# Optimization experiments

Measured on AMD Instinct MI355X. Metric: run time of the kernel, lower is better.

## Reference

```python
import jax, jax.numpy as jnp
import numpy as np

NB_HEAD = 8
SIZE_PER_HEAD = 64
EMB = 512  # word embedding dim; output_dim = NB_HEAD*SIZE_PER_HEAD = 512
B, S = 8, 4096


def setup_inputs() -> dict:
    key = jax.random.key(0)
    ks = jax.random.split(key, 8)
    return {
        "Q_seq": jax.random.normal(ks[0], (B, S, EMB), dtype=jnp.float32),
        "K_seq": jax.random.normal(ks[1], (B, S, EMB), dtype=jnp.float32),
        "V_seq": jax.random.normal(ks[2], (B, S, EMB), dtype=jnp.float32),
        "Q_len": jax.random.randint(ks[3], (B, 1), 0, S, dtype=jnp.int32),
        "V_len": jax.random.randint(ks[4], (B, 1), 0, SIZE_PER_HEAD, dtype=jnp.int32),
        "WQ": jax.random.normal(ks[5], (EMB, NB_HEAD * SIZE_PER_HEAD), dtype=jnp.float32),
        "WK": jax.random.normal(ks[6], (EMB, NB_HEAD * SIZE_PER_HEAD), dtype=jnp.float32),
        "WV": jax.random.normal(ks[7], (EMB, NB_HEAD * SIZE_PER_HEAD), dtype=jnp.float32),
    }


def _proj_heads(x, W):
    # [B,S,E] @ [E,H*d] -> [B,H,S,d]
    y = jnp.einsum('bse,eo->bso', x, W)
    y = y.reshape(y.shape[0], y.shape[1], NB_HEAD, SIZE_PER_HEAD)
    return jnp.transpose(y, (0, 2, 1, 3))


def reference(Q_seq, K_seq, V_seq, Q_len, V_len, WQ, WK, WV):
    H, d = NB_HEAD, SIZE_PER_HEAD
    Q = _proj_heads(Q_seq, WQ)  # [B,H,S,d]
    K = _proj_heads(K_seq, WK)
    V = _proj_heads(V_seq, WV)

    A = (Q * K) / jnp.asarray(d, Q.dtype) ** 0.5  # elementwise, [B,H,S,d]

    # TF code transposes A to [B,d,S,H] and masks along axis 1 (size d) using
    # V_len, then transposes back. Equivalent: additive mask on the LAST axis.
    vmask = jax.nn.one_hot(V_len[:, 0], d, dtype=A.dtype)       # [B,d]
    vmask = 1.0 - jnp.cumsum(vmask, axis=1)                      # [B,d]
    A = A - (1.0 - vmask)[:, None, None, :] * 1e12

    A = jax.nn.softmax(A, axis=-1)  # softmax over d (last axis), as tf.nn.softmax

    O = A * V                              # [B,H,S,d]
    O = jnp.transpose(O, (0, 2, 1, 3))     # [B,S,H,d]
    O = O.reshape(O.shape[0], O.shape[1], H * d)  # [B,S,H*d]

    # multiplicative mask over sequence axis using Q_len
    qmask = jax.nn.one_hot(Q_len[:, 0], O.shape[1], dtype=O.dtype)  # [B,S]
    qmask = 1.0 - jnp.cumsum(qmask, axis=1)
    return O * qmask[:, :, None]
```

## Files before the change

### kernel.cpp

```cpp
#include <hip/hip_runtime.h>

typedef unsigned short u16;
typedef _Float16 f16;
typedef _Float16 f16x4 __attribute__((ext_vector_type(4)));
typedef _Float16 f16x8 __attribute__((ext_vector_type(8)));
typedef float    f32x4 __attribute__((ext_vector_type(4)));

#define BATCH 8
#define SEQ   4096
#define EMB   512
#define NCOL  512

__global__ __launch_bounds__(256) void prep_w(
    const float* __restrict__ Wq, const float* __restrict__ Wk,
    const float* __restrict__ Wv, u16* __restrict__ out)
{
  __shared__ u16 tile[64][65];
  const int z = blockIdx.z;
  const float* in = (z < 2) ? Wq : (z < 4) ? Wk : Wv;
  const bool lo = (z == 1 || z == 3);
  u16* o = out + (size_t)z * EMB * NCOL;
  const int r0 = blockIdx.y * 64, c0 = blockIdx.x * 64;
  const int tx = threadIdx.x, ty = threadIdx.y;
#pragma unroll
  for (int i = 0; i < 16; ++i) {
    const int r = ty * 16 + i;
    const float x = in[(size_t)(r0 + r) * NCOL + (c0 + tx)];
    const f16 h = (f16)x;
    const f16 v = lo ? (f16)((x - (float)h) * 16.0f) : h;
    tile[r][tx] = __builtin_bit_cast(u16, v);
  }
  __syncthreads();
#pragma unroll
  for (int i = 0; i < 16; ++i) {
    const int rr = ty * 16 + i;
    o[(size_t)(c0 + rr) * EMB + (r0 + tx)] = tile[tx][rr];
  }
}

#define PLANE 2048
#define BUFSZ (5*PLANE)

__global__ __launch_bounds__(512, 4) void fused_attn(
    const float* __restrict__ Xq, const float* __restrict__ Xk,
    const float* __restrict__ Xv,
    const int* __restrict__ Qlen, const int* __restrict__ Vlen,
    const u16* __restrict__ Wt,
    float* __restrict__ out)
{
  const int b  = blockIdx.z;
  const int s0 = blockIdx.x * 64;
  const int c0 = blockIdx.y * 128;
  const int qlen = Qlen[b];
  const int t = threadIdx.x;

  if (s0 >= qlen) {
    const f32x4 z4 = {0.f, 0.f, 0.f, 0.f};
#pragma unroll
    for (int it = 0; it < 4; ++it) {
      const int f4  = it * 512 + t;
      const int row = f4 >> 5;
      const int col = (f4 & 31) * 4;
      *(f32x4*)(out + (size_t)(b * SEQ + s0 + row) * NCOL + c0 + col) = z4;
    }
    return;
  }
  const int vlen = Vlen[b];
  const int vl = (vlen == 0) ? 64 : vlen;

  __shared__ f16 smem[2 * BUFSZ] __attribute__((aligned(16)));

  const int w    = t >> 6;
  const int lane = t & 63;
  const int quad = lane >> 4;
  const int l15  = lane & 15;

  const int    srow = t >> 3;
  const int    sj   = t & 7;
  const size_t xg   = (size_t)(b * SEQ + s0 + srow) * EMB + sj * 4;
  const int    swo  = srow * 32 + (((sj >> 1) ^ ((srow >> 1) & 3)) * 8) + (sj & 1) * 4;

  const size_t wb = (size_t)(c0 + w * 16 + l15) * EMB + quad * 8;
  const u16* Wqh_g = Wt                + wb;
  const u16* Wql_g = Wt + 1 * EMB*NCOL + wb;
  const u16* Wkh_g = Wt + 2 * EMB*NCOL + wb;
  const u16* Wkl_g = Wt + 3 * EMB*NCOL + wb;
  const u16* Wv_g  = Wt + 4 * EMB*NCOL + wb;

  const int swz = (l15 >> 1) & 3;
  const int ao  = l15 * 32 + ((quad ^ swz) * 8);

  f32x4 accQ[4], accK[4], accV[4];
#pragma unroll
  for (int rt = 0; rt < 4; ++rt) {
    const f32x4 z = {0.f, 0.f, 0.f, 0.f};
    accQ[rt] = z; accK[rt] = z; accV[rt] = z;
  }

  f32x4 rq, rk, rv;

#define LOADX(TT) do { \
    rq = *(const f32x4*)(Xq + xg + (TT) * 32); \
    rk = *(const f32x4*)(Xk + xg + (TT) * 32); \
    rv = *(const f32x4*)(Xv + xg + (TT) * 32); \
  } while (0)

#define STAGE(BOFS) do { \
    f16* p_ = smem + (BOFS); \
    f16x4 qh_, ql_, kh_, kl_, vh_; \
    _Pragma("unroll") \
    for (int j = 0; j < 4; ++j) { \
      const float xq_ = rq[j]; const f16 qhh_ = (f16)xq_; \
      qh_[j] = qhh_; ql_[j] = (f16)((xq_ - (float)qhh_) * 16.0f); \
      const float xk_ = rk[j]; const f16 khh_ = (f16)xk_; \
      kh_[j] = khh_; kl_[j] = (f16)((xk_ - (float)khh_) * 16.0f); \
      vh_[j] = (f16)rv[j]; \
    } \
    *(f16x4*)(p_ + 0 * PLANE + swo) = qh_; \
    *(f16x4*)(p_ + 1 * PLANE + swo) = ql_; \
    *(f16x4*)(p_ + 2 * PLANE + swo) = kh_; \
    *(f16x4*)(p_ + 3 * PLANE + swo) = kl_; \
    *(f16x4*)(p_ + 4 * PLANE + swo) = vh_; \
  } while (0)

#define COMPUTE(BOFS, KK) do { \
    const f16* p_ = smem + (BOFS); \
    const int kk_ = (KK); \
     \
    { \
      const f16x8 bh_ = *(const f16x8*)(Wqh_g + kk_); \
      const f16x8 bl_ = *(const f16x8*)(Wql_g + kk_); \
      f16x8 b4_; \
      _Pragma("unroll") \
      for (int jj = 0; jj < 8; ++jj) b4_[jj] = bh_[jj] * (f16)0.0625f; \
      _Pragma("unroll") \
      for (int rt = 0; rt < 4; ++rt) { \
        const int ao_ = ao + rt * 512; \
        const f16x8 ah_ = *(const f16x8*)(p_ + 0 * PLANE + ao_); \
        const f16x8 al_ = *(const f16x8*)(p_ + 1 * PLANE + ao_); \
        f16x8 a4_; \
        _Pragma("unroll") \
        for (int jj = 0; jj < 8; ++jj) a4_[jj] = ah_[jj] * (f16)0.0625f; \
        accQ[rt] = __builtin_amdgcn_mfma_f32_16x16x32_f16(ah_, bh_, accQ[rt], 0, 0, 0); \
        accQ[rt] = __builtin_amdgcn_mfma_f32_16x16x32_f16(a4_, bl_, accQ[rt], 0, 0, 0); \
        accQ[rt] = __builtin_amdgcn_mfma_f32_16x16x32_f16(al_, b4_, accQ[rt], 0, 0, 0); \
      } \
    } \
     \
    { \
      const f16x8 bh_ = *(const f16x8*)(Wkh_g + kk_); \
      const f16x8 bl_ = *(const f16x8*)(Wkl_g + kk_); \
      f16x8 b4_; \
      _Pragma("unroll") \
      for (int jj = 0; jj < 8; ++jj) b4_[jj] = bh_[jj] * (f16)0.0625f; \
      _Pragma("unroll") \
      for (int rt = 0; rt < 4; ++rt) { \
        const int ao_ = ao + rt * 512; \
        const f16x8 ah_ = *(const f16x8*)(p_ + 2 * PLANE + ao_); \
        const f16x8 al_ = *(const f16x8*)(p_ + 3 * PLANE + ao_); \
        f16x8 a4_; \
        _Pragma("unroll") \
        for (int jj = 0; jj < 8; ++jj) a4_[jj] = ah_[jj] * (f16)0.0625f; \
        accK[rt] = __builtin_amdgcn_mfma_f32_16x16x32_f16(ah_, bh_, accK[rt], 0, 0, 0); \
        accK[rt] = __builtin_amdgcn_mfma_f32_16x16x32_f16(a4_, bl_, accK[rt], 0, 0, 0); \
        accK[rt] = __builtin_amdgcn_mfma_f32_16x16x32_f16(al_, b4_, accK[rt], 0, 0, 0); \
      } \
    } \
     \
    { \
      const f16x8 bv_ = *(const f16x8*)(Wv_g + kk_); \
      _Pragma("unroll") \
      for (int rt = 0; rt < 4; ++rt) { \
        const f16x8 av_ = *(const f16x8*)(p_ + 4 * PLANE + ao + rt * 512); \
        accV[rt] = __builtin_amdgcn_mfma_f32_16x16x32_f16(av_, bv_, accV[rt], 0, 0, 0); \
      } \
    } \
  } while (0)

  LOADX(0);
  STAGE(0);
  __syncthreads();

#pragma unroll 1
  for (int tt = 0; tt < 16; tt += 2) {
    LOADX(tt + 1);
    COMPUTE(0, tt * 32);
    STAGE(BUFSZ);
    __syncthreads();
    if (tt < 14) LOADX(tt + 2);
    COMPUTE(BUFSZ, (tt + 1) * 32);
    if (tt < 14) STAGE(0);
    __syncthreads();
  }

#undef LOADX
#undef STAGE
#undef COMPUTE

  const float scale = 0.125f;
  float* smf = (float*)smem;

  float eA[4][4];

#pragma unroll
  for (int rt = 0; rt < 4; ++rt) {
#pragma unroll
    for (int r = 0; r < 4; ++r) {
      const float a = accQ[rt][r] * accK[rt][r] * scale;
      const bool msk = ((w & 3) * 16 + l15) < vl;
      float mx = msk ? a : -3.0e38f;
#pragma unroll
      for (int off = 1; off < 16; off <<= 1) mx = fmaxf(mx, __shfl_xor(mx, off));
      const float e = msk ? __expf(a - mx) : 0.0f;
      eA[rt][r] = e;
      float sum = e;
#pragma unroll
      for (int off = 1; off < 16; off <<= 1) sum += __shfl_xor(sum, off);
      const int row = rt * 16 + quad * 4 + r;
      if (l15 == 0) {
        smf[(w * 64 + row) * 2 + 0] = mx;
        smf[(w * 64 + row) * 2 + 1] = sum;
      }
    }
  }
  __syncthreads();

  const int wbase = w & 4;
#pragma unroll
  for (int rt = 0; rt < 4; ++rt) {
#pragma unroll
    for (int r = 0; r < 4; ++r) {
      const int row = rt * 16 + quad * 4 + r;
      const int s   = s0 + row;
      float pm[4], ps[4];
      float M = -3.0e38f;
#pragma unroll
      for (int j = 0; j < 4; ++j) {
        pm[j] = smf[((wbase + j) * 64 + row) * 2 + 0];
        ps[j] = smf[((wbase + j) * 64 + row) * 2 + 1];
        M = fmaxf(M, pm[j]);
      }
      float S = 0.f;
#pragma unroll
      for (int j = 0; j < 4; ++j) S += ps[j] * __expf(pm[j] - M);
      const float qm = (s < qlen) ? 1.0f : 0.0f;
      const float f  = __expf(pm[w & 3] - M) * qm / S;
      const size_t ob = (size_t)(b * SEQ + s) * NCOL + c0 + w * 16 + l15;
      out[ob] = eA[rt][r] * f * accV[rt][r];
    }
  }
}

extern "C" void kernel_launch(void* const* d_in, const int* in_sizes, int n_in,
                              void* d_out, int out_size, void* d_ws, size_t ws_size,
                              hipStream_t stream) {
  const float* Xq   = (const float*)d_in[0];
  const float* Xk   = (const float*)d_in[1];
  const float* Xv   = (const float*)d_in[2];
  const int*   Qlen = (const int*)d_in[3];
  const int*   Vlen = (const int*)d_in[4];
  const float* Wq   = (const float*)d_in[5];
  const float* Wk   = (const float*)d_in[6];
  const float* Wv   = (const float*)d_in[7];
  u16*   Wt  = (u16*)d_ws;
  float* out = (float*)d_out;

  dim3 pg(8, 8, 5), pb(64, 4, 1);
  prep_w<<<pg, pb, 0, stream>>>(Wq, Wk, Wv, Wt);

  dim3 g(SEQ / 64, NCOL / 128, BATCH), blk(512, 1, 1);
  fused_attn<<<g, blk, 0, stream>>>(Xq, Xk, Xv, Qlen, Vlen, Wt, out);
}
```

Before: 372.5 us.

## Use persistent blocks with atomic tile scheduler and drop split-precision rescaling

Turns the fused attention kernel into a persistent-block design: 1024 blocks pull tile indices from a global atomic counter, which is reset by an extra tiny kernel. The goal is to balance load, because tiles past Q_len finish almost immediately while full tiles do all the matmul work. It also removes the ×16 / ×1/16 scaling on the low halves of the split-fp16 operands, which saves the per-iteration vector multiplies and pre-scaled copies. The trade-offs are an extra kernel launch, an atomic and a barrier per tile, and a possible loss of accuracy in the low parts, which may now underflow in fp16.

```diff
diff --git a/kernel.cpp b/kernel.cpp
--- a/kernel.cpp
+++ b/kernel.cpp
@@ -1,6 +1,7 @@
 #include <hip/hip_runtime.h>
 
 typedef unsigned short u16;
+typedef unsigned int   u32;
 typedef _Float16 f16;
 typedef _Float16 f16x4 __attribute__((ext_vector_type(4)));
 typedef _Float16 f16x8 __attribute__((ext_vector_type(8)));
@@ -10,6 +11,7 @@
 #define SEQ   4096
 #define EMB   512
 #define NCOL  512
+#define NTILES 2048
 
 __global__ __launch_bounds__(256) void prep_w(
     const float* __restrict__ Wq, const float* __restrict__ Wk,
@@ -27,7 +29,7 @@
     const int r = ty * 16 + i;
     const float x = in[(size_t)(r0 + r) * NCOL + (c0 + tx)];
     const f16 h = (f16)x;
-    const f16 v = lo ? (f16)((x - (float)h) * 16.0f) : h;
+    const f16 v = lo ? (f16)(x - (float)h) : h;
     tile[r][tx] = __builtin_bit_cast(u16, v);
   }
   __syncthreads();
@@ -38,6 +40,8 @@
   }
 }
 
+__global__ void reset_cnt(u32* cnt) { if (threadIdx.x == 0) *cnt = 0; }
+
 #define PLANE 2048
 #define BUFSZ (5*PLANE)
 
@@ -46,207 +50,200 @@
     const float* __restrict__ Xv,
     const int* __restrict__ Qlen, const int* __restrict__ Vlen,
     const u16* __restrict__ Wt,
-    float* __restrict__ out)
+    float* __restrict__ out, u32* cnt, const int dyn)
 {
-  const int b  = blockIdx.z;
-  const int s0 = blockIdx.x * 64;
-  const int c0 = blockIdx.y * 128;
-  const int qlen = Qlen[b];
   const int t = threadIdx.x;
 
-  if (s0 >= qlen) {
-    const f32x4 z4 = {0.f, 0.f, 0.f, 0.f};
-#pragma unroll
-    for (int it = 0; it < 4; ++it) {
-      const int f4  = it * 512 + t;
-      const int row = f4 >> 5;
-      const int col = (f4 & 31) * 4;
-      *(f32x4*)(out + (size_t)(b * SEQ + s0 + row) * NCOL + c0 + col) = z4;
-    }
-    return;
-  }
-  const int vlen = Vlen[b];
-  const int vl = (vlen == 0) ? 64 : vlen;
-
   __shared__ f16 smem[2 * BUFSZ] __attribute__((aligned(16)));
+  int* slot = (int*)((char*)smem + 2 * BUFSZ * 2 - 4);
 
   const int w    = t >> 6;
   const int lane = t & 63;
   const int quad = lane >> 4;
   const int l15  = lane & 15;
 
-  const int    srow = t >> 3;
-  const int    sj   = t & 7;
-  const size_t xg   = (size_t)(b * SEQ + s0 + srow) * EMB + sj * 4;
-  const int    swo  = srow * 32 + (((sj >> 1) ^ ((srow >> 1) & 3)) * 8) + (sj & 1) * 4;
-
-  const size_t wb = (size_t)(c0 + w * 16 + l15) * EMB + quad * 8;
-  const u16* Wqh_g = Wt                + wb;
-  const u16* Wql_g = Wt + 1 * EMB*NCOL + wb;
-  const u16* Wkh_g = Wt + 2 * EMB*NCOL + wb;
-  const u16* Wkl_g = Wt + 3 * EMB*NCOL + wb;
-  const u16* Wv_g  = Wt + 4 * EMB*NCOL + wb;
+  const int srow = t >> 3;
+  const int sj   = t & 7;
+  const int sk4  = sj * 4;
+  const int swo  = srow * 32 + (((sj >> 1) ^ ((srow >> 1) & 3)) * 8) + (sj & 1) * 4;
 
   const int swz = (l15 >> 1) & 3;
   const int ao  = l15 * 32 + ((quad ^ swz) * 8);
 
-  f32x4 accQ[4], accK[4], accV[4];
-#pragma unroll
-  for (int rt = 0; rt < 4; ++rt) {
-    const f32x4 z = {0.f, 0.f, 0.f, 0.f};
-    accQ[rt] = z; accK[rt] = z; accV[rt] = z;
-  }
-
-  f32x4 rq, rk, rv;
+  const float scale = 0.125f;
+  int tile_static = (int)blockIdx.x;
+
+  for (;;) {
+    if (t == 0) {
+      const int nt = dyn ? (int)atomicAdd(cnt, 1u) : tile_static;
+      tile_static = NTILES;
+      *slot = nt;
+    }
+    __syncthreads();
+    const int tile = __builtin_amdgcn_readfirstlane(*slot);
+    if (tile >= NTILES) break;
+
+    const int s0 = (tile & 63) * 64;
+    const int c0 = ((tile >> 6) & 3) * 128;
+    const int b  = tile >> 8;
+    const int qlen = Qlen[b];
+
+    if (s0 >= qlen) {
+      const f32x4 z4 = {0.f, 0.f, 0.f, 0.f};
+#pragma unroll
+      for (int it = 0; it < 4; ++it) {
+        const int f4  = it * 512 + t;
+        const int row = f4 >> 5;
+        const int col = (f4 & 31) * 4;
+        *(f32x4*)(out + (size_t)(b * SEQ + s0 + row) * NCOL + c0 + col) = z4;
+      }
+      continue;
+    }
+    const int vlen = Vlen[b];
+    const int vl = (vlen == 0) ? 64 : vlen;
+
+    const size_t xg = (size_t)(b * SEQ + s0 + srow) * EMB + sk4;
+    const size_t wb = (size_t)(c0 + w * 16 + l15) * EMB + quad * 8;
+    const u16* Wqh_g = Wt                + wb;
+    const u16* Wql_g = Wt + 1 * EMB*NCOL + wb;
+    const u16* Wkh_g = Wt + 2 * EMB*NCOL + wb;
+    const u16* Wkl_g = Wt + 3 * EMB*NCOL + wb;
+    const u16* Wv_g  = Wt + 4 * EMB*NCOL + wb;
+
+    f32x4 accQ[4], accK[4], accV[4];
+#pragma unroll
+    for (int rt = 0; rt < 4; ++rt) {
+      const f32x4 z = {0.f, 0.f, 0.f, 0.f};
+      accQ[rt] = z; accK[rt] = z; accV[rt] = z;
+    }
+
+    f32x4 rq, rk, rv;
 
 #define LOADX(TT) do { \
-    rq = *(const f32x4*)(Xq + xg + (TT) * 32); \
-    rk = *(const f32x4*)(Xk + xg + (TT) * 32); \
-    rv = *(const f32x4*)(Xv + xg + (TT) * 32); \
-  } while (0)
+      rq = *(const f32x4*)(Xq + xg + (TT) * 32); \
+      rk = *(const f32x4*)(Xk + xg + (TT) * 32); \
+      rv = *(const f32x4*)(Xv + xg + (TT) * 32); \
+    } while (0)
 
 #define STAGE(BOFS) do { \
-    f16* p_ = smem + (BOFS); \
-    f16x4 qh_, ql_, kh_, kl_, vh_; \
-    _Pragma("unroll") \
-    for (int j = 0; j < 4; ++j) { \
-      const float xq_ = rq[j]; const f16 qhh_ = (f16)xq_; \
-      qh_[j] = qhh_; ql_[j] = (f16)((xq_ - (float)qhh_) * 16.0f); \
-      const float xk_ = rk[j]; const f16 khh_ = (f16)xk_; \
-      kh_[j] = khh_; kl_[j] = (f16)((xk_ - (float)khh_) * 16.0f); \
-      vh_[j] = (f16)rv[j]; \
-    } \
-    *(f16x4*)(p_ + 0 * PLANE + swo) = qh_; \
-    *(f16x4*)(p_ + 1 * PLANE + swo) = ql_; \
-    *(f16x4*)(p_ + 2 * PLANE + swo) = kh_; \
-    *(f16x4*)(p_ + 3 * PLANE + swo) = kl_; \
-    *(f16x4*)(p_ + 4 * PLANE + swo) = vh_; \
-  } while (0)
+      f16* p_ = smem + (BOFS); \
+      f16x4 qh_, ql_, kh_, kl_, vh_; \
+      _Pragma("unroll") \
+      for (int j = 0; j < 4; ++j) { \
+        const float xq_ = rq[j]; const f16 qhh_ = (f16)xq_; \
+        qh_[j] = qhh_; ql_[j] = (f16)(xq_ - (float)qhh_); \
+        const float xk_ = rk[j]; const f16 khh_ = (f16)xk_; \
+        kh_[j] = khh_; kl_[j] = (f16)(xk_ - (float)khh_); \
+        vh_[j] = (f16)rv[j]; \
+      } \
+      *(f16x4*)(p_ + 0 * PLANE + swo) = qh_; \
+      *(f16x4*)(p_ + 1 * PLANE + swo) = ql_; \
+      *(f16x4*)(p_ + 2 * PLANE + swo) = kh_; \
+      *(f16x4*)(p_ + 3 * PLANE + swo) = kl_; \
+      *(f16x4*)(p_ + 4 * PLANE + swo) = vh_; \
+    } while (0)
 
 #define COMPUTE(BOFS, KK) do { \
-    const f16* p_ = smem + (BOFS); \
-    const int kk_ = (KK); \
-     \
-    { \
-      const f16x8 bh_ = *(const f16x8*)(Wqh_g + kk_); \
-      const f16x8 bl_ = *(const f16x8*)(Wql_g + kk_); \
-      f16x8 b4_; \
-      _Pragma("unroll") \
-      for (int jj = 0; jj < 8; ++jj) b4_[jj] = bh_[jj] * (f16)0.0625f; \
+      const f16* p_ = smem + (BOFS); \
+      const f16x8 bqh_ = *(const f16x8*)(Wqh_g + (KK)); \
+      const f16x8 bql_ = *(const f16x8*)(Wql_g + (KK)); \
+      const f16x8 bkh_ = *(const f16x8*)(Wkh_g + (KK)); \
+      const f16x8 bkl_ = *(const f16x8*)(Wkl_g + (KK)); \
+      const f16x8 bv_  = *(const f16x8*)(Wv_g  + (KK)); \
       _Pragma("unroll") \
       for (int rt = 0; rt < 4; ++rt) { \
         const int ao_ = ao + rt * 512; \
         const f16x8 ah_ = *(const f16x8*)(p_ + 0 * PLANE + ao_); \
         const f16x8 al_ = *(const f16x8*)(p_ + 1 * PLANE + ao_); \
-        f16x8 a4_; \
-        _Pragma("unroll") \
-        for (int jj = 0; jj < 8; ++jj) a4_[jj] = ah_[jj] * (f16)0.0625f; \
-        accQ[rt] = __builtin_amdgcn_mfma_f32_16x16x32_f16(ah_, bh_, accQ[rt], 0, 0, 0); \
-        accQ[rt] = __builtin_amdgcn_mfma_f32_16x16x32_f16(a4_, bl_, accQ[rt], 0, 0, 0); \
-        accQ[rt] = __builtin_amdgcn_mfma_f32_16x16x32_f16(al_, b4_, accQ[rt], 0, 0, 0); \
-      } \
-    } \
-     \
-    { \
-      const f16x8 bh_ = *(const f16x8*)(Wkh_g + kk_); \
-      const f16x8 bl_ = *(const f16x8*)(Wkl_g + kk_); \
-      f16x8 b4_; \
-      _Pragma("unroll") \
-      for (int jj = 0; jj < 8; ++jj) b4_[jj] = bh_[jj] * (f16)0.0625f; \
+        accQ[rt] = __builtin_amdgcn_mfma_f32_16x16x32_f16(ah_, bqh_, accQ[rt], 0, 0, 0); \
+        accQ[rt] = __builtin_amdgcn_mfma_f32_16x16x32_f16(ah_, bql_, accQ[rt], 0, 0, 0); \
+        accQ[rt] = __builtin_amdgcn_mfma_f32_16x16x32_f16(al_, bqh_, accQ[rt], 0, 0, 0); \
+      } \
       _Pragma("unroll") \
       for (int rt = 0; rt < 4; ++rt) { \
         const int ao_ = ao + rt * 512; \
         const f16x8 ah_ = *(const f16x8*)(p_ + 2 * PLANE + ao_); \
         const f16x8 al_ = *(const f16x8*)(p_ + 3 * PLANE + ao_); \
-        f16x8 a4_; \
-        _Pragma("unroll") \
-        for (int jj = 0; jj < 8; ++jj) a4_[jj] = ah_[jj] * (f16)0.0625f; \
-        accK[rt] = __builtin_amdgcn_mfma_f32_16x16x32_f16(ah_, bh_, accK[rt], 0, 0, 0); \
-        accK[rt] = __builtin_amdgcn_mfma_f32_16x16x32_f16(a4_, bl_, accK[rt], 0, 0, 0); \
-        accK[rt] = __builtin_amdgcn_mfma_f32_16x16x32_f16(al_, b4_, accK[rt], 0, 0, 0); \
-      } \
-    } \
-     \
-    { \
-      const f16x8 bv_ = *(const f16x8*)(Wv_g + kk_); \
+        accK[rt] = __builtin_amdgcn_mfma_f32_16x16x32_f16(ah_, bkh_, accK[rt], 0, 0, 0); \
+        accK[rt] = __builtin_amdgcn_mfma_f32_16x16x32_f16(ah_, bkl_, accK[rt], 0, 0, 0); \
+        accK[rt] = __builtin_amdgcn_mfma_f32_16x16x32_f16(al_, bkh_, accK[rt], 0, 0, 0); \
+      } \
       _Pragma("unroll") \
       for (int rt = 0; rt < 4; ++rt) { \
         const f16x8 av_ = *(const f16x8*)(p_ + 4 * PLANE + ao + rt * 512); \
         accV[rt] = __builtin_amdgcn_mfma_f32_16x16x32_f16(av_, bv_, accV[rt], 0, 0, 0); \
       } \
-    } \
-  } while (0)
-
-  LOADX(0);
-  STAGE(0);
-  __syncthreads();
+    } while (0)
+
+    LOADX(0);
+    STAGE(0);
+    __syncthreads();
 
 #pragma unroll 1
-  for (int tt = 0; tt < 16; tt += 2) {
-    LOADX(tt + 1);
-    COMPUTE(0, tt * 32);
-    STAGE(BUFSZ);
-    __syncthreads();
-    if (tt < 14) LOADX(tt + 2);
-    COMPUTE(BUFSZ, (tt + 1) * 32);
-    if (tt < 14) STAGE(0);
-    __syncthreads();
-  }
+    for (int tt = 0; tt < 16; tt += 2) {
+      LOADX(tt + 1);
+      COMPUTE(0, tt * 32);
+      STAGE(BUFSZ);
+      __syncthreads();
+      if (tt < 14) LOADX(tt + 2);
+      COMPUTE(BUFSZ, (tt + 1) * 32);
+      if (tt < 14) STAGE(0);
+      __syncthreads();
+    }
 
 #undef LOADX
 #undef STAGE
 #undef COMPUTE
 
-  const float scale = 0.125f;
-  float* smf = (float*)smem;
-
-  float eA[4][4];
-
-#pragma unroll
-  for (int rt = 0; rt < 4; ++rt) {
-#pragma unroll
-    for (int r = 0; r < 4; ++r) {
-      const float a = accQ[rt][r] * accK[rt][r] * scale;
-      const bool msk = ((w & 3) * 16 + l15) < vl;
-      float mx = msk ? a : -3.0e38f;
-#pragma unroll
-      for (int off = 1; off < 16; off <<= 1) mx = fmaxf(mx, __shfl_xor(mx, off));
-      const float e = msk ? __expf(a - mx) : 0.0f;
-      eA[rt][r] = e;
-      float sum = e;
-#pragma unroll
-      for (int off = 1; off < 16; off <<= 1) sum += __shfl_xor(sum, off);
-      const int row = rt * 16 + quad * 4 + r;
-      if (l15 == 0) {
-        smf[(w * 64 + row) * 2 + 0] = mx;
-        smf[(w * 64 + row) * 2 + 1] = sum;
+    float* smf = (float*)smem;
+    float eA[4][4];
+
+#pragma unroll
+    for (int rt = 0; rt < 4; ++rt) {
+#pragma unroll
+      for (int r = 0; r < 4; ++r) {
+        const float a = accQ[rt][r] * accK[rt][r] * scale;
+        const bool msk = ((w & 3) * 16 + l15) < vl;
+        float mx = msk ? a : -3.0e38f;
+#pragma unroll
+        for (int off = 1; off < 16; off <<= 1) mx = fmaxf(mx, __shfl_xor(mx, off));
+        const float e = msk ? __expf(a - mx) : 0.0f;
+        eA[rt][r] = e;
+        float sum = e;
+#pragma unroll
+        for (int off = 1; off < 16; off <<= 1) sum += __shfl_xor(sum, off);
+        const int row = rt * 16 + quad * 4 + r;
+        if (l15 == 0) {
+          smf[(w * 64 + row) * 2 + 0] = mx;
+          smf[(w * 64 + row) * 2 + 1] = sum;
+        }
       }
     }
-  }
-  __syncthreads();
-
-  const int wbase = w & 4;
-#pragma unroll
-  for (int rt = 0; rt < 4; ++rt) {
-#pragma unroll
-    for (int r = 0; r < 4; ++r) {
-      const int row = rt * 16 + quad * 4 + r;
-      const int s   = s0 + row;
-      float pm[4], ps[4];
-      float M = -3.0e38f;
-#pragma unroll
-      for (int j = 0; j < 4; ++j) {
-        pm[j] = smf[((wbase + j) * 64 + row) * 2 + 0];
-        ps[j] = smf[((wbase + j) * 64 + row) * 2 + 1];
-        M = fmaxf(M, pm[j]);
+    __syncthreads();
+
+    const int wbase = w & 4;
+#pragma unroll
+    for (int rt = 0; rt < 4; ++rt) {
+#pragma unroll
+      for (int r = 0; r < 4; ++r) {
+        const int row = rt * 16 + quad * 4 + r;
+        const int s   = s0 + row;
+        float pm[4], ps[4];
+        float M = -3.0e38f;
+#pragma unroll
+        for (int j = 0; j < 4; ++j) {
+          pm[j] = smf[((wbase + j) * 64 + row) * 2 + 0];
+          ps[j] = smf[((wbase + j) * 64 + row) * 2 + 1];
+          M = fmaxf(M, pm[j]);
+        }
+        float S = 0.f;
+#pragma unroll
+        for (int j = 0; j < 4; ++j) S += ps[j] * __expf(pm[j] - M);
+        const float qm = (s < qlen) ? 1.0f : 0.0f;
+        const float f  = __expf(pm[w & 3] - M) * qm / S;
+        const size_t ob = (size_t)(b * SEQ + s) * NCOL + c0 + w * 16 + l15;
+        out[ob] = eA[rt][r] * f * accV[rt][r];
       }
-      float S = 0.f;
-#pragma unroll
-      for (int j = 0; j < 4; ++j) S += ps[j] * __expf(pm[j] - M);
-      const float qm = (s < qlen) ? 1.0f : 0.0f;
-      const float f  = __expf(pm[w & 3] - M) * qm / S;
-      const size_t ob = (size_t)(b * SEQ + s) * NCOL + c0 + w * 16 + l15;
-      out[ob] = eA[rt][r] * f * accV[rt][r];
     }
   }
 }
@@ -265,9 +262,14 @@
   u16*   Wt  = (u16*)d_ws;
   float* out = (float*)d_out;
 
+  const size_t wt_bytes = (size_t)5 * EMB * NCOL * sizeof(u16);
+  u32* cnt = (u32*)((char*)d_ws + wt_bytes);
+  const int dyn = (ws_size >= wt_bytes + sizeof(u32)) ? 1 : 0;
+
   dim3 pg(8, 8, 5), pb(64, 4, 1);
   prep_w<<<pg, pb, 0, stream>>>(Wq, Wk, Wv, Wt);
-
-  dim3 g(SEQ / 64, NCOL / 128, BATCH), blk(512, 1, 1);
-  fused_attn<<<g, blk, 0, stream>>>(Xq, Xk, Xv, Qlen, Vlen, Wt, out);
+  if (dyn) reset_cnt<<<1, 64, 0, stream>>>(cnt);
+
+  dim3 g(dyn ? 1024 : NTILES, 1, 1), blk(512, 1, 1);
+  fused_attn<<<g, blk, 0, stream>>>(Xq, Xk, Xv, Qlen, Vlen, Wt, out, cnt, dyn);
 }
```

Measured after the change: 328.1 us. -11.9%, faster.
